# Performance work log

Measured on AMD Instinct MI355X. Metric: run time of the kernel, lower is better.

Reference implementation:

```python
import jax, jax.numpy as jnp
import numpy as np

N, M, P, H = 200000, 20, 64, 256
EPS = 1e-12  # inside sqrt: avoids NaN grads when duplicate neighbors give zero distance


def setup_inputs() -> dict:
    key = jax.random.key(0)
    ks = jax.random.split(key, 8)
    x = jax.random.normal(ks[0], (N, P), jnp.float32)
    pos = jax.random.uniform(ks[1], (N, 2), jnp.float32) * 10.0
    y = jax.random.normal(ks[2], (N,), jnp.float32)
    # m distinct-from-self neighbor indices per node (offset trick avoids self loops)
    off = jax.random.randint(ks[3], (N, M), 1, N)
    nbr_idx = ((jnp.arange(N)[:, None] + off) % N).astype(jnp.int32)
    theta = jnp.array([1.0, 1.0, 0.1], jnp.float32)  # (sigma_sq, phi, tau)
    w1 = jax.random.normal(ks[4], (P, H), jnp.float32) * (1.0 / np.sqrt(P))
    b1 = jnp.zeros((H,), jnp.float32)
    w2 = jax.random.normal(ks[5], (H, 1), jnp.float32) * (1.0 / np.sqrt(H))
    b2 = jnp.zeros((1,), jnp.float32)
    return dict(x=x, pos=pos, y=y, nbr_idx=nbr_idx, theta=theta,
                w1=w1, b1=b1, w2=w2, b2=b2)


def _dist(a, b):
    return jnp.sqrt(jnp.sum((a - b) ** 2, axis=-1) + EPS)


def reference(x, pos, y, nbr_idx, theta, w1, b1, w2, b2):
    sigma_sq, phi, tau = theta[0], theta[1], theta[2]
    tau_sq = tau * sigma_sq
    m = nbr_idx.shape[1]
    pos_nbr = pos[nbr_idx]                                            # [N,M,2] gather
    # Cov(i, N(i)): exponential covariance of node-to-neighbor distances  [N,M]
    cov_i_ni = sigma_sq * jnp.exp(-phi * _dist(pos[:, None, :], pos_nbr))
    # Cov(N(i), N(i)) + nugget on the diagonal                          [N,M,M]
    d_nn = _dist(pos_nbr[:, :, None, :], pos_nbr[:, None, :, :])
    cov = sigma_sq * jnp.exp(-phi * d_nn) + tau_sq * jnp.eye(m, dtype=pos.dtype)
    # B_i = Cov(N,N)^{-1} Cov(i,N)  (batched small solve == inv @ vec)  [N,M]
    b_i = jnp.linalg.solve(cov, cov_i_ni[..., None])[..., 0]
    f_i = sigma_sq + tau - jnp.sum(b_i * cov_i_ni, axis=1)             # [N]
    inv_sqrt_f = 1.0 / jnp.sqrt(f_i)
    # MLP: Linear -> ReLU -> Linear, squeezed to [N]
    o = (jax.nn.relu(x @ w1 + b1) @ w2 + b2)[:, 0]
    y_decor = (y - jnp.sum(y[nbr_idx] * b_i, axis=1)) * inv_sqrt_f
    o_decor = (o - jnp.sum(o[nbr_idx] * b_i, axis=1)) * inv_sqrt_f
    return (y_decor, o_decor, o)
```

## Files before the change

### kernel.cpp

```cpp
#include <hip/hip_runtime.h>


#define MM   20
#define PP   64
#define HH   256
#define EPSF 1e-12f

#define CSE(j, r) csx[2*(j)*((j)+1) + (r)]
#define C20(r)    csx[60 + (r)]

typedef __attribute__((ext_vector_type(8))) short bf16x8;
typedef __attribute__((ext_vector_type(4))) float f32x4;

static __device__ __forceinline__ unsigned short f2bf(float f) {
    unsigned int u = __builtin_bit_cast(unsigned int, f);
    u += 0x7fffu + ((u >> 16) & 1u);
    return (unsigned short)(u >> 16);
}
static __device__ __forceinline__ float bf2f(unsigned short h) {
    unsigned int u = ((unsigned int)h) << 16;
    return __builtin_bit_cast(float, u);
}

__global__ __launch_bounds__(256, 2)
void mlp_mfma_kernel(const float* __restrict__ x,
                     const float* __restrict__ w1,
                     const float* __restrict__ b1,
                     const float* __restrict__ w2,
                     const float* __restrict__ b2,
                     float* __restrict__ o_out, int n)
{
    __shared__ __align__(16) short swh[PP * HH];
    __shared__ __align__(16) short swl[PP * HH];
    const int tid = threadIdx.x;

    {
        const int col = tid;
        const int t = col >> 4, nn = col & 15;
        #pragma unroll
        for (int g = 0; g < 8; ++g) {
            const int s = g >> 2, q = g & 3;
            bf16x8 hv, lv;
            #pragma unroll
            for (int u = 0; u < 8; ++u) {
                float v = w1[(g * 8 + u) * HH + col];
                unsigned short h = f2bf(v);
                hv[u] = (short)h;
                lv[u] = (short)f2bf(v - bf2f(h));
            }
            const int base = ((((t * 2 + s) * 4 + q) * 16) + nn) * 8;
            *(bf16x8*)&swh[base] = hv;
            *(bf16x8*)&swl[base] = lv;
        }
    }
    __syncthreads();

    const int lane = tid & 63;
    const int wv   = tid >> 6;
    const int nn   = lane & 15;
    const int q    = lane >> 4;
    const int wb   = blockIdx.x * 256 + wv * 64;

    float w2v[16], b1v[16];
    #pragma unroll
    for (int t = 0; t < 16; ++t) {
        w2v[t] = w2[t * 16 + nn];
        b1v[t] = b1[t * 16 + nn];
    }

    bf16x8 ah[4][2], al[4][2];
    #pragma unroll
    for (int mt = 0; mt < 4; ++mt) {
        const int row = wb + mt * 16 + nn;
        #pragma unroll
        for (int s = 0; s < 2; ++s) {
            float v[8];
            if (row < n) {
                const float* xp = x + (size_t)row * PP + s * 32 + q * 8;
                float4 va = *(const float4*)(xp);
                float4 vb = *(const float4*)(xp + 4);
                v[0]=va.x; v[1]=va.y; v[2]=va.z; v[3]=va.w;
                v[4]=vb.x; v[5]=vb.y; v[6]=vb.z; v[7]=vb.w;
            } else {
                #pragma unroll
                for (int u = 0; u < 8; ++u) v[u] = 0.0f;
            }
            bf16x8 h, l;
            #pragma unroll
            for (int u = 0; u < 8; ++u) {
                unsigned short hb = f2bf(v[u]);
                h[u] = (short)hb;
                l[u] = (short)f2bf(v[u] - bf2f(hb));
            }
            ah[mt][s] = h;
            al[mt][s] = l;
        }
    }

    float part[4][4];
    #pragma unroll
    for (int mt = 0; mt < 4; ++mt)
        #pragma unroll
        for (int r = 0; r < 4; ++r) part[mt][r] = 0.0f;

    #pragma unroll
    for (int t = 0; t < 16; ++t) {
        f32x4 acc[4];
        #pragma unroll
        for (int mt = 0; mt < 4; ++mt) acc[mt] = (f32x4)(0.0f);
        #pragma unroll
        for (int s = 0; s < 2; ++s) {
            const int fb = ((((t * 2 + s) * 4 + q) * 16) + nn) * 8;
            bf16x8 bh = *(const bf16x8*)&swh[fb];
            bf16x8 bl = *(const bf16x8*)&swl[fb];
            #pragma unroll
            for (int mt = 0; mt < 4; ++mt) {
                acc[mt] = __builtin_amdgcn_mfma_f32_16x16x32_bf16(ah[mt][s], bh, acc[mt], 0, 0, 0);
                acc[mt] = __builtin_amdgcn_mfma_f32_16x16x32_bf16(al[mt][s], bh, acc[mt], 0, 0, 0);
                acc[mt] = __builtin_amdgcn_mfma_f32_16x16x32_bf16(ah[mt][s], bl, acc[mt], 0, 0, 0);
            }
        }
        #pragma unroll
        for (int mt = 0; mt < 4; ++mt)
            #pragma unroll
            for (int r = 0; r < 4; ++r)
                part[mt][r] = fmaf(fmaxf(acc[mt][r] + b1v[t], 0.0f), w2v[t], part[mt][r]);
    }

    #pragma unroll
    for (int w = 1; w < 16; w <<= 1)
        #pragma unroll
        for (int mt = 0; mt < 4; ++mt)
            #pragma unroll
            for (int r = 0; r < 4; ++r)
                part[mt][r] += __shfl_xor(part[mt][r], w, 64);

    const float bb = b2[0];
    if (nn == 0) {
        #pragma unroll
        for (int mt = 0; mt < 4; ++mt) {
            const int row = wb + mt * 16 + q * 4;
            if (row < n) {
                float4 o4 = make_float4(part[mt][0] + bb, part[mt][1] + bb,
                                        part[mt][2] + bb, part[mt][3] + bb);
                *(float4*)&o_out[row] = o4;
            }
        }
    }
}

#define QSWZ(v, s) __builtin_bit_cast(float, __builtin_amdgcn_ds_swizzle( \
    __builtin_bit_cast(int, (v)), 0x8000 | (0x55 * (s))))

__global__ __launch_bounds__(256, 2)
void solve_kernel(const float* __restrict__ pos,
                  const float* __restrict__ y,
                  const int*   __restrict__ nbr,
                  const float* __restrict__ theta,
                  const float* __restrict__ o_in,
                  float* __restrict__ yd,
                  float* __restrict__ od, int n)
{
    const int tid  = threadIdx.x;
    const int h_   = tid & 3;
    const int i    = blockIdx.x * 64 + (tid >> 2);
    if (i >= n) return;

    const float sigma_sq = theta[0];
    const float phi      = theta[1];
    const float tau      = theta[2];
    const float tau_sq   = tau * sigma_sq;

    const float L2E = 1.44269504088896340736f;
    const float c1  = -phi * L2E;
    const float c0  = __builtin_amdgcn_logf(sigma_sq);

    const float sqrtEPS = __builtin_amdgcn_sqrtf(EPSF);
    const float diagA   = __builtin_amdgcn_exp2f(fmaf(sqrtEPS, c1, c0)) + tau_sq;
    const float diagB   = sigma_sq + tau;

    int idx[MM];
    const int4* nb4 = (const int4*)(nbr + (size_t)i * MM);
    #pragma unroll
    for (int k = 0; k < MM / 4; ++k) {
        int4 v = nb4[k];
        idx[4*k] = v.x; idx[4*k+1] = v.y; idx[4*k+2] = v.z; idx[4*k+3] = v.w;
    }

    float px[21], py[21];
    const float2* pos2 = (const float2*)pos;
    #pragma unroll
    for (int j = 0; j < MM; ++j) {
        float2 p = pos2[idx[j]];
        px[j] = p.x; py[j] = p.y;
    }
    {
        float2 p = pos2[i];
        px[20] = p.x; py[20] = p.y;
    }

    float cx[5], cy[5];
    #pragma unroll
    for (int j = 0; j < 5; ++j) {
        int cj = nbr[(size_t)i * MM + 4*j + h_];
        float2 p = pos2[cj];
        cx[j] = p.x; cy[j] = p.y;
    }

    float bv[21];
    {
        const float* src = (h_ & 1) ? o_in : y;
        #pragma unroll
        for (int j = 0; j < MM; ++j) bv[j] = src[idx[j]];
        bv[20] = src[i];
    }

    float csx[81];
    #pragma unroll
    for (int j = 0; j < 5; ++j) {
        #pragma unroll
        for (int r = 0; r <= 4*j + 3; ++r) {
            float dx = px[r] - cx[j];
            float dy = py[r] - cy[j];
            float d  = __builtin_amdgcn_sqrtf(fmaf(dx, dx, fmaf(dy, dy, EPSF)));
            float v  = __builtin_amdgcn_exp2f(fmaf(d, c1, c0));
            v = (r == 4*j + h_) ? diagA : v;
            CSE(j, r) = v;
        }
    }
    #pragma unroll
    for (int r = 0; r < 20; ++r) {
        float dx = px[r] - px[20];
        float dy = py[r] - py[20];
        float d  = __builtin_amdgcn_sqrtf(fmaf(dx, dx, fmaf(dy, dy, EPSF)));
        C20(r)   = __builtin_amdgcn_exp2f(fmaf(d, c1, c0));
    }
    C20(20) = diagB;

    float pk[5], p20, pbv, pd;
    #pragma unroll 1
    for (int k = 0; k < 20; ++k) {
        switch (k) {
#define CASEK(K) case K: {                                                 \
            _Pragma("unroll")                                              \
            for (int j = 0; j < 5; ++j)                                    \
                pk[j] = (4*j + 3 >= (K)) ? CSE(j, (K)) : 0.0f;             \
            p20 = C20(K); pbv = bv[K];                                     \
            pd  = QSWZ(pk[(K) >> 2], (K) & 3);                             \
        } break;
        CASEK(0)  CASEK(1)  CASEK(2)  CASEK(3)  CASEK(4)
        CASEK(5)  CASEK(6)  CASEK(7)  CASEK(8)  CASEK(9)
        CASEK(10) CASEK(11) CASEK(12) CASEK(13) CASEK(14)
        CASEK(15) CASEK(16) CASEK(17) CASEK(18) CASEK(19)
#undef CASEK
        default: break;
        }
        float rp = __builtin_amdgcn_rcpf(pd);
        rp = rp * (2.0f - pd * rp);

        float mv[5];
        #pragma unroll
        for (int j = 0; j < 5; ++j)
            mv[j] = (4*j + h_ > k) ? pk[j] * rp : 0.0f;

        float mall[21];
#define GATHER(R) mall[R] = QSWZ(mv[(R) >> 2], (R) & 3);
        GATHER(0)  GATHER(1)  GATHER(2)  GATHER(3)  GATHER(4)
        GATHER(5)  GATHER(6)  GATHER(7)  GATHER(8)  GATHER(9)
        GATHER(10) GATHER(11) GATHER(12) GATHER(13) GATHER(14)
        GATHER(15) GATHER(16) GATHER(17) GATHER(18) GATHER(19)
#undef GATHER
        mall[20] = p20 * rp;

        #pragma unroll
        for (int j = 0; j < 5; ++j) {
            float pkj = pk[j];
            #pragma unroll
            for (int r = 0; r <= 4*j + 3; ++r)
                CSE(j, r) = fmaf(-mall[r], pkj, CSE(j, r));
        }
        #pragma unroll
        for (int r = 0; r <= 20; ++r) {
            C20(r) = fmaf(-mall[r], p20, C20(r));
            bv[r]  = fmaf(-mall[r], pbv, bv[r]);
        }
    }

    float f  = C20(20);
    float is = __builtin_amdgcn_rsqf(f);
    is = is * fmaf(-0.5f * f * is, is, 1.5f);

    if (h_ == 0)      yd[i] = bv[20] * is;
    else if (h_ == 1) od[i] = bv[20] * is;
}

extern "C" void kernel_launch(void* const* d_in, const int* in_sizes, int n_in,
                              void* d_out, int out_size, void* d_ws, size_t ws_size,
                              hipStream_t stream)
{
    const float* x     = (const float*)d_in[0];
    const float* pos   = (const float*)d_in[1];
    const float* y     = (const float*)d_in[2];
    const int*   nbr   = (const int*)  d_in[3];
    const float* theta = (const float*)d_in[4];
    const float* w1    = (const float*)d_in[5];
    const float* b1    = (const float*)d_in[6];
    const float* w2    = (const float*)d_in[7];
    const float* b2    = (const float*)d_in[8];

    const int n = in_sizes[2];
    float* out = (float*)d_out;
    float* yd = out;
    float* od = out + (size_t)n;
    float* oo = out + 2 * (size_t)n;

    mlp_mfma_kernel<<<(n + 255) / 256, 256, 0, stream>>>(x, w1, b1, w2, b2, oo, n);
    solve_kernel<<<(n + 63) / 64, 256, 0, stream>>>(pos, y, nbr, theta, oo, yd, od, n);
}
```

Measured before the change: 215.1 us.

## Split elimination loop into blocked phases skipping eliminated columns; persistent MLP grid

The Gaussian elimination loop in the solve kernel is split into five phases of four pivots each. Each phase only touches column blocks and rows at or beyond the current block, so it skips multiply-adds on entries that were already eliminated and shrinks the per-iteration swizzle gather count. The MLP kernel becomes a grid-stride persistent kernel capped at 512 blocks, so the bf16 split of W1 into shared memory is done once per block rather than once per 256-row tile. Code size grows, and the capped grid may reduce latency hiding.

```diff
diff --git a/kernel.cpp b/kernel.cpp
--- a/kernel.cpp
+++ b/kernel.cpp
@@ -28,7 +28,7 @@
                      const float* __restrict__ b1,
                      const float* __restrict__ w2,
                      const float* __restrict__ b2,
-                     float* __restrict__ o_out, int n)
+                     float* __restrict__ o_out, int n, int ntiles)
 {
     __shared__ __align__(16) short swh[PP * HH];
     __shared__ __align__(16) short swl[PP * HH];
@@ -59,7 +59,6 @@
     const int wv   = tid >> 6;
     const int nn   = lane & 15;
     const int q    = lane >> 4;
-    const int wb   = blockIdx.x * 256 + wv * 64;
 
     float w2v[16], b1v[16];
     #pragma unroll
@@ -67,83 +66,87 @@
         w2v[t] = w2[t * 16 + nn];
         b1v[t] = b1[t * 16 + nn];
     }
-
-    bf16x8 ah[4][2], al[4][2];
-    #pragma unroll
-    for (int mt = 0; mt < 4; ++mt) {
-        const int row = wb + mt * 16 + nn;
-        #pragma unroll
-        for (int s = 0; s < 2; ++s) {
-            float v[8];
-            if (row < n) {
-                const float* xp = x + (size_t)row * PP + s * 32 + q * 8;
-                float4 va = *(const float4*)(xp);
-                float4 vb = *(const float4*)(xp + 4);
-                v[0]=va.x; v[1]=va.y; v[2]=va.z; v[3]=va.w;
-                v[4]=vb.x; v[5]=vb.y; v[6]=vb.z; v[7]=vb.w;
-            } else {
+    const float bb = b2[0];
+
+    for (int tile = blockIdx.x; tile < ntiles; tile += gridDim.x) {
+        const int wb = tile * 256 + wv * 64;
+
+        bf16x8 ah[4][2], al[4][2];
+        #pragma unroll
+        for (int mt = 0; mt < 4; ++mt) {
+            const int row = wb + mt * 16 + nn;
+            #pragma unroll
+            for (int s = 0; s < 2; ++s) {
+                float v[8];
+                if (row < n) {
+                    const float* xp = x + (size_t)row * PP + s * 32 + q * 8;
+                    float4 va = *(const float4*)(xp);
+                    float4 vb = *(const float4*)(xp + 4);
+                    v[0]=va.x; v[1]=va.y; v[2]=va.z; v[3]=va.w;
+                    v[4]=vb.x; v[5]=vb.y; v[6]=vb.z; v[7]=vb.w;
+                } else {
+                    #pragma unroll
+                    for (int u = 0; u < 8; ++u) v[u] = 0.0f;
+                }
+                bf16x8 h, l;
                 #pragma unroll
-                for (int u = 0; u < 8; ++u) v[u] = 0.0f;
+                for (int u = 0; u < 8; ++u) {
+                    unsigned short hb = f2bf(v[u]);
+                    h[u] = (short)hb;
+                    l[u] = (short)f2bf(v[u] - bf2f(hb));
+                }
+                ah[mt][s] = h;
+                al[mt][s] = l;
             }
-            bf16x8 h, l;
-            #pragma unroll
-            for (int u = 0; u < 8; ++u) {
-                unsigned short hb = f2bf(v[u]);
-                h[u] = (short)hb;
-                l[u] = (short)f2bf(v[u] - bf2f(hb));
+        }
+
+        float part[4][4];
+        #pragma unroll
+        for (int mt = 0; mt < 4; ++mt)
+            #pragma unroll
+            for (int r = 0; r < 4; ++r) part[mt][r] = 0.0f;
+
+        #pragma unroll
+        for (int t = 0; t < 16; ++t) {
+            f32x4 acc[4];
+            #pragma unroll
+            for (int mt = 0; mt < 4; ++mt) acc[mt] = (f32x4)(0.0f);
+            #pragma unroll
+            for (int s = 0; s < 2; ++s) {
+                const int fb = ((((t * 2 + s) * 4 + q) * 16) + nn) * 8;
+                bf16x8 bh = *(const bf16x8*)&swh[fb];
+                bf16x8 bl = *(const bf16x8*)&swl[fb];
+                #pragma unroll
+                for (int mt = 0; mt < 4; ++mt) {
+                    acc[mt] = __builtin_amdgcn_mfma_f32_16x16x32_bf16(ah[mt][s], bh, acc[mt], 0, 0, 0);
+                    acc[mt] = __builtin_amdgcn_mfma_f32_16x16x32_bf16(al[mt][s], bh, acc[mt], 0, 0, 0);
+                    acc[mt] = __builtin_amdgcn_mfma_f32_16x16x32_bf16(ah[mt][s], bl, acc[mt], 0, 0, 0);
+                }
             }
-            ah[mt][s] = h;
-            al[mt][s] = l;
-        }
-    }
-
-    float part[4][4];
-    #pragma unroll
-    for (int mt = 0; mt < 4; ++mt)
-        #pragma unroll
-        for (int r = 0; r < 4; ++r) part[mt][r] = 0.0f;
-
-    #pragma unroll
-    for (int t = 0; t < 16; ++t) {
-        f32x4 acc[4];
-        #pragma unroll
-        for (int mt = 0; mt < 4; ++mt) acc[mt] = (f32x4)(0.0f);
-        #pragma unroll
-        for (int s = 0; s < 2; ++s) {
-            const int fb = ((((t * 2 + s) * 4 + q) * 16) + nn) * 8;
-            bf16x8 bh = *(const bf16x8*)&swh[fb];
-            bf16x8 bl = *(const bf16x8*)&swl[fb];
+            #pragma unroll
+            for (int mt = 0; mt < 4; ++mt)
+                #pragma unroll
+                for (int r = 0; r < 4; ++r)
+                    part[mt][r] = fmaf(fmaxf(acc[mt][r] + b1v[t], 0.0f), w2v[t], part[mt][r]);
+        }
+
+        #pragma unroll
+        for (int w = 1; w < 16; w <<= 1)
+            #pragma unroll
+            for (int mt = 0; mt < 4; ++mt)
+                #pragma unroll
+                for (int r = 0; r < 4; ++r)
+                    part[mt][r] += __shfl_xor(part[mt][r], w, 64);
+
+        if (nn == 0) {
             #pragma unroll
             for (int mt = 0; mt < 4; ++mt) {
-                acc[mt] = __builtin_amdgcn_mfma_f32_16x16x32_bf16(ah[mt][s], bh, acc[mt], 0, 0, 0);
-                acc[mt] = __builtin_amdgcn_mfma_f32_16x16x32_bf16(al[mt][s], bh, acc[mt], 0, 0, 0);
-                acc[mt] = __builtin_amdgcn_mfma_f32_16x16x32_bf16(ah[mt][s], bl, acc[mt], 0, 0, 0);
-            }
-        }
-        #pragma unroll
-        for (int mt = 0; mt < 4; ++mt)
-            #pragma unroll
-            for (int r = 0; r < 4; ++r)
-                part[mt][r] = fmaf(fmaxf(acc[mt][r] + b1v[t], 0.0f), w2v[t], part[mt][r]);
-    }
-
-    #pragma unroll
-    for (int w = 1; w < 16; w <<= 1)
-        #pragma unroll
-        for (int mt = 0; mt < 4; ++mt)
-            #pragma unroll
-            for (int r = 0; r < 4; ++r)
-                part[mt][r] += __shfl_xor(part[mt][r], w, 64);
-
-    const float bb = b2[0];
-    if (nn == 0) {
-        #pragma unroll
-        for (int mt = 0; mt < 4; ++mt) {
-            const int row = wb + mt * 16 + q * 4;
-            if (row < n) {
-                float4 o4 = make_float4(part[mt][0] + bb, part[mt][1] + bb,
-                                        part[mt][2] + bb, part[mt][3] + bb);
-                *(float4*)&o_out[row] = o4;
+                const int row = wb + mt * 16 + q * 4;
+                if (row < n) {
+                    float4 o4 = make_float4(part[mt][0] + bb, part[mt][1] + bb,
+                                            part[mt][2] + bb, part[mt][3] + bb);
+                    *(float4*)&o_out[row] = o4;
+                }
             }
         }
     }
@@ -151,6 +154,15 @@
 
 #define QSWZ(v, s) __builtin_bit_cast(float, __builtin_amdgcn_ds_swizzle( \
     __builtin_bit_cast(int, (v)), 0x8000 | (0x55 * (s))))
+
+#define GATH(R) mall[R] = QSWZ(mv[(R) >> 2], (R) & 3);
+
+#define SCASE(K, P) case K: {                                              \
+    _Pragma("unroll")                                                      \
+    for (int j = (P); j < 5; ++j) pk[j] = CSE(j, (K));                     \
+    p20 = C20(K); pbv = bv[K];                                             \
+    pd  = QSWZ(pk[(P)], (K) & 3);                                          \
+} break;
 
 __global__ __launch_bounds__(256, 2)
 void solve_kernel(const float* __restrict__ pos,
@@ -237,41 +249,23 @@
     }
     C20(20) = diagB;
 
-    float pk[5], p20, pbv, pd;
+    float pk[5], mv[5], mall[21], p20, pbv, pd;
+
     #pragma unroll 1
-    for (int k = 0; k < 20; ++k) {
+    for (int k = 0; k < 4; ++k) {
         switch (k) {
-#define CASEK(K) case K: {                                                 \
-            _Pragma("unroll")                                              \
-            for (int j = 0; j < 5; ++j)                                    \
-                pk[j] = (4*j + 3 >= (K)) ? CSE(j, (K)) : 0.0f;             \
-            p20 = C20(K); pbv = bv[K];                                     \
-            pd  = QSWZ(pk[(K) >> 2], (K) & 3);                             \
-        } break;
-        CASEK(0)  CASEK(1)  CASEK(2)  CASEK(3)  CASEK(4)
-        CASEK(5)  CASEK(6)  CASEK(7)  CASEK(8)  CASEK(9)
-        CASEK(10) CASEK(11) CASEK(12) CASEK(13) CASEK(14)
-        CASEK(15) CASEK(16) CASEK(17) CASEK(18) CASEK(19)
-#undef CASEK
+        SCASE(0,0) SCASE(1,0) SCASE(2,0) SCASE(3,0)
         default: break;
         }
         float rp = __builtin_amdgcn_rcpf(pd);
         rp = rp * (2.0f - pd * rp);
-
-        float mv[5];
         #pragma unroll
         for (int j = 0; j < 5; ++j)
             mv[j] = (4*j + h_ > k) ? pk[j] * rp : 0.0f;
-
-        float mall[21];
-#define GATHER(R) mall[R] = QSWZ(mv[(R) >> 2], (R) & 3);
-        GATHER(0)  GATHER(1)  GATHER(2)  GATHER(3)  GATHER(4)
-        GATHER(5)  GATHER(6)  GATHER(7)  GATHER(8)  GATHER(9)
-        GATHER(10) GATHER(11) GATHER(12) GATHER(13) GATHER(14)
-        GATHER(15) GATHER(16) GATHER(17) GATHER(18) GATHER(19)
-#undef GATHER
+        GATH(0)  GATH(1)  GATH(2)  GATH(3)  GATH(4)  GATH(5)  GATH(6)
+        GATH(7)  GATH(8)  GATH(9)  GATH(10) GATH(11) GATH(12) GATH(13)
+        GATH(14) GATH(15) GATH(16) GATH(17) GATH(18) GATH(19)
         mall[20] = p20 * rp;
-
         #pragma unroll
         for (int j = 0; j < 5; ++j) {
             float pkj = pk[j];
@@ -281,6 +275,115 @@
         }
         #pragma unroll
         for (int r = 0; r <= 20; ++r) {
+            C20(r) = fmaf(-mall[r], p20, C20(r));
+            bv[r]  = fmaf(-mall[r], pbv, bv[r]);
+        }
+    }
+
+    #pragma unroll 1
+    for (int k = 4; k < 8; ++k) {
+        switch (k) {
+        SCASE(4,1) SCASE(5,1) SCASE(6,1) SCASE(7,1)
+        default: break;
+        }
+        float rp = __builtin_amdgcn_rcpf(pd);
+        rp = rp * (2.0f - pd * rp);
+        #pragma unroll
+        for (int j = 1; j < 5; ++j)
+            mv[j] = (4*j + h_ > k) ? pk[j] * rp : 0.0f;
+        GATH(4)  GATH(5)  GATH(6)  GATH(7)  GATH(8)  GATH(9)  GATH(10)
+        GATH(11) GATH(12) GATH(13) GATH(14) GATH(15) GATH(16) GATH(17)
+        GATH(18) GATH(19)
+        mall[20] = p20 * rp;
+        #pragma unroll
+        for (int j = 1; j < 5; ++j) {
+            float pkj = pk[j];
+            #pragma unroll
+            for (int r = 4; r <= 4*j + 3; ++r)
+                CSE(j, r) = fmaf(-mall[r], pkj, CSE(j, r));
+        }
+        #pragma unroll
+        for (int r = 4; r <= 20; ++r) {
+            C20(r) = fmaf(-mall[r], p20, C20(r));
+            bv[r]  = fmaf(-mall[r], pbv, bv[r]);
+        }
+    }
+
+    #pragma unroll 1
+    for (int k = 8; k < 12; ++k) {
+        switch (k) {
+        SCASE(8,2) SCASE(9,2) SCASE(10,2) SCASE(11,2)
+        default: break;
+        }
+        float rp = __builtin_amdgcn_rcpf(pd);
+        rp = rp * (2.0f - pd * rp);
+        #pragma unroll
+        for (int j = 2; j < 5; ++j)
+            mv[j] = (4*j + h_ > k) ? pk[j] * rp : 0.0f;
+        GATH(8)  GATH(9)  GATH(10) GATH(11) GATH(12) GATH(13) GATH(14)
+        GATH(15) GATH(16) GATH(17) GATH(18) GATH(19)
+        mall[20] = p20 * rp;
+        #pragma unroll
+        for (int j = 2; j < 5; ++j) {
+            float pkj = pk[j];
+            #pragma unroll
+            for (int r = 8; r <= 4*j + 3; ++r)
+                CSE(j, r) = fmaf(-mall[r], pkj, CSE(j, r));
+        }
+        #pragma unroll
+        for (int r = 8; r <= 20; ++r) {
+            C20(r) = fmaf(-mall[r], p20, C20(r));
+            bv[r]  = fmaf(-mall[r], pbv, bv[r]);
+        }
+    }
+
+    #pragma unroll 1
+    for (int k = 12; k < 16; ++k) {
+        switch (k) {
+        SCASE(12,3) SCASE(13,3) SCASE(14,3) SCASE(15,3)
+        default: break;
+        }
+        float rp = __builtin_amdgcn_rcpf(pd);
+        rp = rp * (2.0f - pd * rp);
+        #pragma unroll
+        for (int j = 3; j < 5; ++j)
+            mv[j] = (4*j + h_ > k) ? pk[j] * rp : 0.0f;
+        GATH(12) GATH(13) GATH(14) GATH(15) GATH(16) GATH(17) GATH(18)
+        GATH(19)
+        mall[20] = p20 * rp;
+        #pragma unroll
+        for (int j = 3; j < 5; ++j) {
+            float pkj = pk[j];
+            #pragma unroll
+            for (int r = 12; r <= 4*j + 3; ++r)
+                CSE(j, r) = fmaf(-mall[r], pkj, CSE(j, r));
+        }
+        #pragma unroll
+        for (int r = 12; r <= 20; ++r) {
+            C20(r) = fmaf(-mall[r], p20, C20(r));
+            bv[r]  = fmaf(-mall[r], pbv, bv[r]);
+        }
+    }
+
+    #pragma unroll 1
+    for (int k = 16; k < 20; ++k) {
+        switch (k) {
+        SCASE(16,4) SCASE(17,4) SCASE(18,4) SCASE(19,4)
+        default: break;
+        }
+        float rp = __builtin_amdgcn_rcpf(pd);
+        rp = rp * (2.0f - pd * rp);
+        mv[4] = (16 + h_ > k) ? pk[4] * rp : 0.0f;
+        GATH(16) GATH(17) GATH(18) GATH(19)
+        mall[20] = p20 * rp;
+        {
+            float pkj = pk[4];
+            #pragma unroll
+            for (int r = 16; r <= 19; ++r)
+                CSE(4, r) = fmaf(-mall[r], pkj, CSE(4, r));
+        }
+        #pragma unroll
+        for (int r = 16; r <= 20; ++r) {
             C20(r) = fmaf(-mall[r], p20, C20(r));
             bv[r]  = fmaf(-mall[r], pbv, bv[r]);
         }
@@ -314,6 +417,8 @@
     float* od = out + (size_t)n;
     float* oo = out + 2 * (size_t)n;
 
-    mlp_mfma_kernel<<<(n + 255) / 256, 256, 0, stream>>>(x, w1, b1, w2, b2, oo, n);
+    const int ntiles = (n + 255) / 256;
+    const int grid1  = ntiles < 512 ? ntiles : 512;
+    mlp_mfma_kernel<<<grid1, 256, 0, stream>>>(x, w1, b1, w2, b2, oo, n, ntiles);
     solve_kernel<<<(n + 63) / 64, 256, 0, stream>>>(pos, y, nbr, theta, oo, yd, od, n);
 }
```

Result: slower. 264.6 us (+23.0%).
